# Performance work log

Measured on AMD Instinct MI355X. Metric: run time of the kernel, lower is better.

Reference implementation:

```python
import jax, jax.numpy as jnp
import numpy as np

B, S, D = 8, 4096, 192
MEM_READ, MEM_WRITE, MEM_READY = 156, 157, 158


def setup_inputs() -> dict:
    key = jax.random.key(0)
    ks = jax.random.split(key, 9)
    inp = {"x": jax.random.normal(ks[0], (B, S, D), dtype=jnp.float32)}
    names = ["Wq_r", "Wk_r", "Wv_r", "Wo_r", "Wq_w", "Wk_w", "Wv_w", "Wo_w"]
    for i, n in enumerate(names):
        inp[n] = jax.random.normal(ks[i + 1], (D, D), dtype=jnp.float32) * 0.02
    return inp


def _attention(x, Wq, Wk, Wv, Wo):
    # single-head, non-causal PureAttention: q/k/v = x @ W.T, softmax(qk^T/sqrt(D)) v, then W_o
    q = jnp.einsum('bsd,ed->bse', x, Wq)
    k = jnp.einsum('bsd,ed->bse', x, Wk)
    v = jnp.einsum('bsd,ed->bse', x, Wv)
    scale = jnp.asarray(1.0 / np.sqrt(D), x.dtype)
    scores = jnp.einsum('bqe,bke->bqk', q, k) * scale  # [B,S,S]
    attn = jax.nn.softmax(scores, axis=-1)
    o = jnp.einsum('bqk,bke->bqe', attn, v)
    return jnp.einsum('bse,oe->bso', o, Wo)


def reference(x, Wq_r, Wk_r, Wv_r, Wo_r, Wq_w, Wk_w, Wv_w, Wo_w):
    read_flag = x[:, 0, MEM_READ]    # [B]
    write_flag = x[:, 0, MEM_WRITE]  # [B]
    read_res = _attention(x, Wq_r, Wk_r, Wv_r, Wo_r)
    write_res = _attention(x, Wq_w, Wk_w, Wv_w, Wo_w)
    rg = read_flag[:, None, None]
    wg = write_flag[:, None, None]
    out = x + rg * (read_res - x) + wg * (write_res - x)
    out = out.at[:, :, MEM_READ].set(0.0)
    out = out.at[:, :, MEM_WRITE].set(0.0)
    ready = (read_flag + write_flag)[:, None]  # broadcast over seq
    out = out.at[:, :, MEM_READY].set(jnp.broadcast_to(ready, out.shape[:2]))
    return out
```

## Files before the change

kernel.cpp:

```cpp
#include <hip/hip_runtime.h>
#include <stdint.h>

#define B_ 8
#define S_ 4096
#define D_ 192
#define M_ (B_*S_)

typedef short v8s __attribute__((ext_vector_type(8)));
typedef float v4f __attribute__((ext_vector_type(4)));
typedef unsigned short v4us __attribute__((ext_vector_type(4)));

static __device__ __forceinline__ unsigned short f2bf(float f){
  union{float f; unsigned u;} v; v.f=f;
  unsigned u = v.u;
  unsigned r = (u + 0x7fffu + ((u>>16)&1u))>>16;
  return (unsigned short)r;
}
static __device__ __forceinline__ float fexp2(float x){
  return __builtin_amdgcn_exp2f(x);
}
static __device__ __forceinline__ unsigned cvtpk(float lo, float hi){
  unsigned r;
  asm("v_cvt_pk_bf16_f32 %0, %1, %2" : "=v"(r) : "v"(lo), "v"(hi));
  return r;
}

typedef const __attribute__((address_space(1))) unsigned int gu32;
typedef __attribute__((address_space(3))) unsigned int lu32;
#define GLL16(gp, lp) __builtin_amdgcn_global_load_lds((gu32*)(gp), (lu32*)(lp), 16, 0, 0)

__global__ void cvt_w_kernel(const float* w0,const float* w1,const float* w2,const float* w3,
                             const float* w4,const float* w5,const float* w6,const float* w7,
                             unsigned short* dst){
  int w = blockIdx.y;
  const float* src;
  switch(w){
    case 0: src=w0; break; case 1: src=w1; break; case 2: src=w2; break; case 3: src=w3; break;
    case 4: src=w4; break; case 5: src=w5; break; case 6: src=w6; break; default: src=w7; break;
  }
  int i = blockIdx.x*256 + threadIdx.x;
  float v = src[i];
  if(w==0 || w==4) v *= 0.10411754211316668f;
  dst[(size_t)w*36864 + i] = f2bf(v);
}

__global__ __launch_bounds__(256) void proj_kernel(
    const float* __restrict__ x, const unsigned short* __restrict__ Wb,
    unsigned short* __restrict__ QKV)
{
  __shared__ __align__(16) unsigned short Vstage[192*72];
  const size_t MD = (size_t)M_*D_;
  int tid = threadIdx.x;
  int wid = tid>>6, lane = tid&63;
  int lr = lane&15, lg = lane>>4, kb = lg*8;
  int m0 = blockIdx.x*64 + wid*16;
  int row = m0 + lr;

  v8s a[6];
  #pragma unroll
  for(int c=0;c<6;c++){
    const float* xp = &x[(size_t)row*D_ + c*32 + kb];
    float4 f0 = *(const float4*)xp;
    float4 f1 = *(const float4*)(xp+4);
    v8s t;
    t[0]=(short)f2bf(f0.x); t[1]=(short)f2bf(f0.y); t[2]=(short)f2bf(f0.z); t[3]=(short)f2bf(f0.w);
    t[4]=(short)f2bf(f1.x); t[5]=(short)f2bf(f1.y); t[6]=(short)f2bf(f1.z); t[7]=(short)f2bf(f1.w);
    a[c]=t;
  }
  int bidx = m0 / S_;
  int sb   = (blockIdx.x*64) % S_;
  int sloc = wid*16 + lg*4;

  for(int path=0; path<2; path++){
    unsigned short* dstQ = QKV + (size_t)path*3*MD;
    for(int which=0; which<2; which++){
      const unsigned short* W = Wb + (size_t)(path*4 + which)*36864;
      unsigned short* dst = which==0 ? dstQ : dstQ + MD;
      #pragma unroll
      for(int nt=0; nt<12; nt++){
        v4f acc = {0.f,0.f,0.f,0.f};
        int n = nt*16 + lr;
        #pragma unroll
        for(int c=0;c<6;c++){
          v8s bfr = *(const v8s*)&W[(size_t)n*D_ + c*32 + kb];
          acc = __builtin_amdgcn_mfma_f32_16x16x32_bf16(a[c], bfr, acc, 0,0,0);
        }
        int col = nt*16 + lr;
        int r0 = m0 + lg*4;
        #pragma unroll
        for(int r=0;r<4;r++) dst[(size_t)(r0+r)*D_ + col] = f2bf(acc[r]);
      }
    }
    {
      const unsigned short* W = Wb + (size_t)(path*4 + 2)*36864;
      #pragma unroll
      for(int nt=0; nt<12; nt++){
        v4f acc = {0.f,0.f,0.f,0.f};
        int n = nt*16 + lr;
        #pragma unroll
        for(int c=0;c<6;c++){
          v8s bfr = *(const v8s*)&W[(size_t)n*D_ + c*32 + kb];
          acc = __builtin_amdgcn_mfma_f32_16x16x32_bf16(a[c], bfr, acc, 0,0,0);
        }
        int col = nt*16 + lr;
        v4us pk;
        pk[0]=f2bf(acc[0]); pk[1]=f2bf(acc[1]); pk[2]=f2bf(acc[2]); pk[3]=f2bf(acc[3]);
        *(v4us*)&Vstage[col*72 + sloc] = pk;
      }
      __syncthreads();
      unsigned short* dstV = dstQ + 2*MD;
      size_t vg = (size_t)bidx*D_*S_ + sb;
      #pragma unroll
      for(int j=0;j<6;j++){
        int i = tid + j*256;
        int d = i>>3, s8 = (i&7)*8;
        *(v8s*)&dstV[vg + (size_t)d*S_ + s8] = *(const v8s*)&Vstage[d*72 + s8];
      }
      __syncthreads();
    }
  }
}

__global__ __launch_bounds__(512,3) void attn_kernel(unsigned short* __restrict__ QKV)
{
  __shared__ __align__(16) unsigned short Kb[2][32*192];
  __shared__ __align__(16) unsigned short Vb[3][192*32];

  int flat = blockIdx.x + 32*blockIdx.y + 256*blockIdx.z;
  int w = (flat&7)*64 + (flat>>3);
  int qi = w & 31;
  int b  = (w>>5) & 7;
  int z  = w>>8;

  const size_t MD = (size_t)M_*D_;
  size_t poff = (size_t)z*3*MD;
  const unsigned short* Q  = QKV + poff;
  const unsigned short* K  = QKV + poff + MD;
  const unsigned short* Vt = QKV + poff + 2*MD;
  unsigned short* O = QKV + poff;

  int q0 = qi*128;
  int tid = threadIdx.x, wid=tid>>6, lane=tid&63;
  int lr = lane&15, lg = lane>>4, kb = lg*8;
  size_t bbase = (size_t)b*S_*D_;
  const size_t vbase = (size_t)b*D_*S_;
  int qrow0 = q0 + wid*16;

  bool isK = wid < 4;
  int cb = (isK ? wid : wid-4)*3;
  int soff[3];
  #pragma unroll
  for(int j=0;j<3;j++){
    int pb = (cb+j)*1024 + lane*16;
    if(isK){
      int krow = pb/384, kin = pb%384;
      soff[j] = krow*192 + ((kin ^ ((krow&7)<<4))>>1);
    } else {
      int vrow = pb>>6,  vin = pb&63;
      soff[j] = vrow*4096 + ((vin ^ (((vrow>>1)&3)<<4))>>1);
    }
  }
  int xk = (lr&7)<<4;
  int kco[6];
  #pragma unroll
  for(int c=0;c<6;c++) kco[c] = ((c*64 + lg*16) ^ xk) >> 1;
  int vro = ((lg*16) ^ (((lr>>1)&3)<<4)) >> 1;

  v8s qf[6];
  {
    size_t qrow = bbase + (size_t)(qrow0 + lr)*D_;
    #pragma unroll
    for(int c=0;c<6;c++) qf[c] = *(const v8s*)&Q[qrow + c*32 + kb];
  }
  float lsum = 0.f;
  v4f oacc[12];
  #pragma unroll
  for(int e=0;e<12;e++) oacc[e] = (v4f){0.f,0.f,0.f,0.f};

  auto stage = [&](int t, int kbuf, int vbuf){
    if(isK){
      const unsigned short* kg = K + bbase + (size_t)t*6144;
      #pragma unroll
      for(int j=0;j<3;j++) GLL16(kg + soff[j], &Kb[kbuf][(cb+j)*512]);
    } else {
      const unsigned short* vg = Vt + vbase + (size_t)t*32;
      #pragma unroll
      for(int j=0;j<3;j++) GLL16(vg + soff[j], &Vb[vbuf][(cb+j)*512]);
    }
  };
  auto do_qk = [&](int kcur, v4f sacc[2]){
    __builtin_amdgcn_s_setprio(1);
    #pragma unroll
    for(int ct=0; ct<2; ct++){
      v4f s = {0.f,0.f,0.f,0.f};
      #pragma unroll
      for(int c=0;c<6;c++){
        v8s kf = *(const v8s*)&Kb[kcur][(ct*16+lr)*192 + kco[c]];
        s = __builtin_amdgcn_mfma_f32_16x16x32_bf16(kf, qf[c], s, 0,0,0);
      }
      sacc[ct]=s;
    }
    __builtin_amdgcn_s_setprio(0);
  };
  auto do_softmax = [&](v4f sacc[2], v8s& pa){
    float p00=fexp2(sacc[0][0]), p01=fexp2(sacc[0][1]);
    float p02=fexp2(sacc[0][2]), p03=fexp2(sacc[0][3]);
    float p10=fexp2(sacc[1][0]), p11=fexp2(sacc[1][1]);
    float p12=fexp2(sacc[1][2]), p13=fexp2(sacc[1][3]);
    lsum += ((p00+p01)+(p02+p03)) + ((p10+p11)+(p12+p13));
    unsigned X0=cvtpk(p00,p01), X1=cvtpk(p02,p03);
    unsigned Y0=cvtpk(p10,p11), Y1=cvtpk(p12,p13);
    asm("v_permlane32_swap_b32 %0, %1" : "+v"(Y0), "+v"(X0));
    asm("v_permlane32_swap_b32 %0, %1" : "+v"(Y1), "+v"(X1));
    asm("v_permlane16_swap_b32 %0, %1" : "+v"(Y0), "+v"(X0));
    asm("v_permlane16_swap_b32 %0, %1" : "+v"(Y1), "+v"(X1));
    union{ v8s s; unsigned w[4]; } u;
    u.w[0] = X0;  u.w[1] = X1;  u.w[2] = Y0;  u.w[3] = Y1;
    pa = u.s;
  };
  auto do_pv = [&](int vcur, v8s pa){
    __builtin_amdgcn_s_setprio(1);
    #pragma unroll
    for(int e=0;e<12;e++){
      v8s vbf = *(const v8s*)&Vb[vcur][(e*16+lr)*32 + vro];
      oacc[e] = __builtin_amdgcn_mfma_f32_16x16x32_bf16(pa, vbf, oacc[e], 0,0,0);
    }
    __builtin_amdgcn_s_setprio(0);
  };

  stage(0, 0, 0);
  asm volatile("s_waitcnt vmcnt(0)" ::: "memory");
  __syncthreads();

  v8s pa_prev;
  {
    v4f sacc[2];
    do_qk(0, sacc);
    stage(1, 1, 1);
    __builtin_amdgcn_sched_barrier(0);
    do_softmax(sacc, pa_prev);
  }

  for(int t=1; t<128; t++){
    asm volatile("s_waitcnt vmcnt(0)" ::: "memory");
    __syncthreads();
    v4f sacc[2];
    do_qk(t&1, sacc);
    if(t<127) stage(t+1, (t+1)&1, (t+1)%3);
    __builtin_amdgcn_sched_barrier(0);
    do_pv((t-1)%3, pa_prev);
    do_softmax(sacc, pa_prev);
  }
  do_pv(127%3, pa_prev);

  float ps = lsum;
  ps += __shfl_xor(ps, 16);
  ps += __shfl_xor(ps, 32);
  float iv = 1.0f/ps;
  float invr[4];
  #pragma unroll
  for(int r=0;r<4;r++) invr[r] = __shfl(iv, lg*4+r, 16);
  size_t orow0 = bbase + (size_t)(qrow0 + lg*4)*D_;
  #pragma unroll
  for(int e=0;e<12;e++){
    #pragma unroll
    for(int r=0;r<4;r++){
      O[orow0 + (size_t)r*D_ + e*16 + lr] = f2bf(oacc[e][r]*invr[r]);
    }
  }
}

__global__ __launch_bounds__(256) void final_kernel(
  const float* __restrict__ x,
  const unsigned short* __restrict__ Or,
  const unsigned short* __restrict__ Ow,
  const unsigned short* __restrict__ WoR,
  const unsigned short* __restrict__ WoW,
  float* __restrict__ out)
{
  int tid=threadIdx.x, wid=tid>>6, lane=tid&63;
  int lr=lane&15, lg=lane>>4, kb=lg*8;
  int m0 = blockIdx.x*64 + wid*16;
  int arow = m0 + lr;
  v8s ar[6], aw[6];
  #pragma unroll
  for(int c=0;c<6;c++){
    ar[c] = *(const v8s*)&Or[(size_t)arow*D_ + c*32 + kb];
    aw[c] = *(const v8s*)&Ow[(size_t)arow*D_ + c*32 + kb];
  }
  int bidx = m0 / S_;
  float rf = x[(size_t)bidx*S_*D_ + 156];
  float wf = x[(size_t)bidx*S_*D_ + 157];
  #pragma unroll
  for(int nt=0; nt<12; nt++){
    v4f accR={0.f,0.f,0.f,0.f}, accW={0.f,0.f,0.f,0.f};
    int n = nt*16 + lr;
    #pragma unroll
    for(int c=0;c<6;c++){
      v8s br = *(const v8s*)&WoR[(size_t)n*D_ + c*32 + kb];
      accR = __builtin_amdgcn_mfma_f32_16x16x32_bf16(ar[c], br, accR,0,0,0);
      v8s bw = *(const v8s*)&WoW[(size_t)n*D_ + c*32 + kb];
      accW = __builtin_amdgcn_mfma_f32_16x16x32_bf16(aw[c], bw, accW,0,0,0);
    }
    #pragma unroll
    for(int r=0;r<4;r++){
      int row = m0 + lg*4 + r;
      int col = nt*16 + lr;
      float xv = x[(size_t)row*D_ + col];
      float val = xv + rf*(accR[r]-xv) + wf*(accW[r]-xv);
      if(col==156||col==157) val = 0.f;
      else if(col==158) val = rf+wf;
      out[(size_t)row*D_ + col] = val;
    }
  }
}

extern "C" void kernel_launch(void* const* d_in, const int* in_sizes, int n_in,
                              void* d_out, int out_size, void* d_ws, size_t ws_size,
                              hipStream_t stream) {
  const float* x = (const float*)d_in[0];
  unsigned short* ws = (unsigned short*)d_ws;
  const size_t WSZ = 36864;
  const size_t MD  = (size_t)M_*D_;
  unsigned short* Wb  = ws;
  unsigned short* QKV = ws + 8*WSZ;

  cvt_w_kernel<<<dim3(144,8),256,0,stream>>>(
      (const float*)d_in[1],(const float*)d_in[2],(const float*)d_in[3],(const float*)d_in[4],
      (const float*)d_in[5],(const float*)d_in[6],(const float*)d_in[7],(const float*)d_in[8], Wb);

  proj_kernel<<<512,256,0,stream>>>(x, Wb, QKV);
  attn_kernel<<<dim3(32,8,2),512,0,stream>>>(QKV);
  final_kernel<<<512,256,0,stream>>>(x, QKV , QKV+3*MD ,
                                     Wb+3*WSZ, Wb+7*WSZ, (float*)d_out);
}
```

Baseline: 356.8 us.

## Switch attention Q/K/V and probabilities to FP8 MFMA

Projections now write Q, K and V as FP8 bytes, with the softmax scale split evenly across Wq and Wk. The attention kernel uses 16x16x32 FP8 MFMAs for both QK and PV, and repacks the softmax probabilities to FP8. This halves the Q/K/V memory traffic and LDS footprint and uses higher-throughput FP8 matrix instructions. The LDS staging is reorganised and outputs go to a separate bf16 buffer. The cost is a large loss of precision in the scores and probabilities, plus extra conversion work in softmax.

```diff
diff --git a/kernel.cpp b/kernel.cpp
--- a/kernel.cpp
+++ b/kernel.cpp
@@ -8,7 +8,6 @@
 
 typedef short v8s __attribute__((ext_vector_type(8)));
 typedef float v4f __attribute__((ext_vector_type(4)));
-typedef unsigned short v4us __attribute__((ext_vector_type(4)));
 
 static __device__ __forceinline__ unsigned short f2bf(float f){
   union{float f; unsigned u;} v; v.f=f;
@@ -23,6 +22,37 @@
   unsigned r;
   asm("v_cvt_pk_bf16_f32 %0, %1, %2" : "=v"(r) : "v"(lo), "v"(hi));
   return r;
+}
+static __device__ __forceinline__ float asf(unsigned u){
+  union{unsigned u; float f;} v; v.u=u; return v.f;
+}
+
+static __device__ __forceinline__ unsigned sw_fp8(float x){
+  union{float f; unsigned u;} v; v.f = x;
+  unsigned s = (v.u >> 24) & 0x80u;
+  float a = fabsf(x);
+  if (a < 0.001953125f) return s;
+  if (a >= 240.f) return s | 0x7Eu;
+  if (a < 0.015625f) {
+    int m = (int)(a*512.f + 0.5f); if(m>7) m=7;
+    return s | (unsigned)m;
+  }
+  int e = (int)((v.u >> 23) & 0xff) - 127;
+  unsigned mant = (v.u >> 20) & 0x7u;
+  unsigned rest = v.u & 0xFFFFFu;
+  if (rest > 0x80000u || (rest == 0x80000u && (mant&1u))) mant++;
+  unsigned ee = (unsigned)(e + 7);
+  if (mant == 8u){ mant = 0u; ee++; }
+  return s | (ee<<3) | mant;
+}
+template<bool HI>
+static __device__ __forceinline__ unsigned pk8(float a, float b, unsigned old){
+#if __has_builtin(__builtin_amdgcn_cvt_pk_fp8_f32)
+  return __builtin_amdgcn_cvt_pk_fp8_f32(a, b, old, HI);
+#else
+  unsigned p = sw_fp8(a) | (sw_fp8(b)<<8);
+  return HI ? ((old & 0x0000FFFFu) | (p<<16)) : ((old & 0xFFFF0000u) | p);
+#endif
 }
 
 typedef const __attribute__((address_space(1))) unsigned int gu32;
@@ -40,16 +70,16 @@
   }
   int i = blockIdx.x*256 + threadIdx.x;
   float v = src[i];
-  if(w==0 || w==4) v *= 0.10411754211316668f;
+  if(w==0 || w==4 || w==1 || w==5) v *= 0.32267249f;
   dst[(size_t)w*36864 + i] = f2bf(v);
 }
 
 __global__ __launch_bounds__(256) void proj_kernel(
     const float* __restrict__ x, const unsigned short* __restrict__ Wb,
-    unsigned short* __restrict__ QKV)
+    unsigned char* __restrict__ QKV8)
 {
-  __shared__ __align__(16) unsigned short Vstage[192*72];
-  const size_t MD = (size_t)M_*D_;
+  __shared__ __align__(16) unsigned char Vstage[192*80];
+  const size_t MDB = (size_t)M_*D_;
   int tid = threadIdx.x;
   int wid = tid>>6, lane = tid&63;
   int lr = lane&15, lg = lane>>4, kb = lg*8;
@@ -72,10 +102,10 @@
   int sloc = wid*16 + lg*4;
 
   for(int path=0; path<2; path++){
-    unsigned short* dstQ = QKV + (size_t)path*3*MD;
+    unsigned char* dstQ = QKV8 + (size_t)path*3*MDB;
     for(int which=0; which<2; which++){
       const unsigned short* W = Wb + (size_t)(path*4 + which)*36864;
-      unsigned short* dst = which==0 ? dstQ : dstQ + MD;
+      unsigned char* dst = which==0 ? dstQ : dstQ + MDB;
       #pragma unroll
       for(int nt=0; nt<12; nt++){
         v4f acc = {0.f,0.f,0.f,0.f};
@@ -88,7 +118,10 @@
         int col = nt*16 + lr;
         int r0 = m0 + lg*4;
         #pragma unroll
-        for(int r=0;r<4;r++) dst[(size_t)(r0+r)*D_ + col] = f2bf(acc[r]);
+        for(int r=0;r<4;r++){
+          unsigned p = pk8<false>(acc[r], 0.f, 0u);
+          dst[(size_t)(r0+r)*D_ + col] = (unsigned char)(p & 0xFF);
+        }
       }
     }
     {
@@ -103,28 +136,29 @@
           acc = __builtin_amdgcn_mfma_f32_16x16x32_bf16(a[c], bfr, acc, 0,0,0);
         }
         int col = nt*16 + lr;
-        v4us pk;
-        pk[0]=f2bf(acc[0]); pk[1]=f2bf(acc[1]); pk[2]=f2bf(acc[2]); pk[3]=f2bf(acc[3]);
-        *(v4us*)&Vstage[col*72 + sloc] = pk;
+        unsigned pk4 = pk8<false>(acc[0], acc[1], 0u);
+        pk4 = pk8<true>(acc[2], acc[3], pk4);
+        *(unsigned*)&Vstage[col*80 + sloc] = pk4;
       }
       __syncthreads();
-      unsigned short* dstV = dstQ + 2*MD;
+      unsigned char* dstV = dstQ + 2*MDB;
       size_t vg = (size_t)bidx*D_*S_ + sb;
       #pragma unroll
-      for(int j=0;j<6;j++){
+      for(int j=0;j<3;j++){
         int i = tid + j*256;
-        int d = i>>3, s8 = (i&7)*8;
-        *(v8s*)&dstV[vg + (size_t)d*S_ + s8] = *(const v8s*)&Vstage[d*72 + s8];
+        int d = i>>2, ci = (i&3)*16;
+        *(v8s*)&dstV[vg + (size_t)d*S_ + ci] = *(const v8s*)&Vstage[d*80 + ci];
       }
       __syncthreads();
     }
   }
 }
 
-__global__ __launch_bounds__(512,3) void attn_kernel(unsigned short* __restrict__ QKV)
+__global__ __launch_bounds__(512,3) void attn_kernel(const unsigned char* __restrict__ QKV8,
+                                                     unsigned short* __restrict__ Ob)
 {
-  __shared__ __align__(16) unsigned short Kb[2][32*192];
-  __shared__ __align__(16) unsigned short Vb[3][192*32];
+  __shared__ __align__(16) unsigned char KL[2*8192];
+  __shared__ __align__(16) unsigned char VL[3*9216];
 
   int flat = blockIdx.x + 32*blockIdx.y + 256*blockIdx.z;
   int w = (flat&7)*64 + (flat>>3);
@@ -132,45 +166,41 @@
   int b  = (w>>5) & 7;
   int z  = w>>8;
 
-  const size_t MD = (size_t)M_*D_;
-  size_t poff = (size_t)z*3*MD;
-  const unsigned short* Q  = QKV + poff;
-  const unsigned short* K  = QKV + poff + MD;
-  const unsigned short* Vt = QKV + poff + 2*MD;
-  unsigned short* O = QKV + poff;
+  const size_t MDB = (size_t)M_*D_;
+  const unsigned char* Q8 = QKV8 + (size_t)z*3*MDB;
+  const unsigned char* K8 = Q8 + MDB;
+  const unsigned char* V8 = Q8 + 2*MDB;
+  unsigned short* O = Ob + (size_t)z*M_*D_;
 
   int q0 = qi*128;
   int tid = threadIdx.x, wid=tid>>6, lane=tid&63;
-  int lr = lane&15, lg = lane>>4, kb = lg*8;
-  size_t bbase = (size_t)b*S_*D_;
-  const size_t vbase = (size_t)b*D_*S_;
+  int lr = lane&15, lg = lane>>4;
+  size_t bK = (size_t)b*S_*D_;
+  size_t bV = (size_t)b*D_*S_;
   int qrow0 = q0 + wid*16;
 
-  bool isK = wid < 4;
-  int cb = (isK ? wid : wid-4)*3;
-  int soff[3];
-  #pragma unroll
-  for(int j=0;j<3;j++){
-    int pb = (cb+j)*1024 + lane*16;
-    if(isK){
-      int krow = pb/384, kin = pb%384;
-      soff[j] = krow*192 + ((kin ^ ((krow&7)<<4))>>1);
-    } else {
-      int vrow = pb>>6,  vin = pb&63;
-      soff[j] = vrow*4096 + ((vin ^ (((vrow>>1)&3)<<4))>>1);
-    }
-  }
-  int xk = (lr&7)<<4;
-  int kco[6];
-  #pragma unroll
-  for(int c=0;c<6;c++) kco[c] = ((c*64 + lg*16) ^ xk) >> 1;
-  int vro = ((lg*16) ^ (((lr>>1)&3)<<4)) >> 1;
-
-  v8s qf[6];
+  int krow = tid>>4, kpc = (tid&15)<<4;
+  int kg = kpc ^ ((krow&7)<<4);
+  int kSrc = krow*192 + (kg<192 ? kg : 176);
+  int kLds = tid*16;
+  int vd0 = tid/3,        vq0 = (tid%3)<<4;
+  int vSrc0 = vd0*S_ + (vq0<32 ? vq0 : 16);
+  int vLds0 = tid*16;
+  int vc1 = tid+512;
+  int vd1 = vc1/3,        vq1 = (vc1%3)<<4;
+  int vSrc1 = vd1*S_ + (vq1<32 ? vq1 : 16);
+  int vLds1 = vc1*16;
+  bool v2 = tid < 64;
+
+  int kro[6];
+  #pragma unroll
+  for(int c=0;c<6;c++) kro[c] = (c*32 + lg*8) ^ ((lr&7)<<4);
+
+  long qf8[6];
   {
-    size_t qrow = bbase + (size_t)(qrow0 + lr)*D_;
-    #pragma unroll
-    for(int c=0;c<6;c++) qf[c] = *(const v8s*)&Q[qrow + c*32 + kb];
+    const unsigned char* qp = Q8 + bK + (size_t)(qrow0 + lr)*D_;
+    #pragma unroll
+    for(int c=0;c<6;c++) qf8[c] = *(const long*)(qp + c*32 + lg*8);
   }
   float lsum = 0.f;
   v4f oacc[12];
@@ -178,31 +208,29 @@
   for(int e=0;e<12;e++) oacc[e] = (v4f){0.f,0.f,0.f,0.f};
 
   auto stage = [&](int t, int kbuf, int vbuf){
-    if(isK){
-      const unsigned short* kg = K + bbase + (size_t)t*6144;
-      #pragma unroll
-      for(int j=0;j<3;j++) GLL16(kg + soff[j], &Kb[kbuf][(cb+j)*512]);
-    } else {
-      const unsigned short* vg = Vt + vbase + (size_t)t*32;
-      #pragma unroll
-      for(int j=0;j<3;j++) GLL16(vg + soff[j], &Vb[vbuf][(cb+j)*512]);
-    }
+    const unsigned char* Kg = K8 + bK + (size_t)t*6144;
+    const unsigned char* Vg = V8 + bV + (size_t)t*32;
+    GLL16(Kg + kSrc, KL + kbuf*8192 + kLds);
+    GLL16(Vg + vSrc0, VL + vbuf*9216 + vLds0);
+    if(v2) GLL16(Vg + vSrc1, VL + vbuf*9216 + vLds1);
   };
   auto do_qk = [&](int kcur, v4f sacc[2]){
+    const unsigned char* KB = KL + kcur*8192;
     __builtin_amdgcn_s_setprio(1);
     #pragma unroll
     for(int ct=0; ct<2; ct++){
       v4f s = {0.f,0.f,0.f,0.f};
+      const unsigned char* rb = KB + (ct*16+lr)*256;
       #pragma unroll
       for(int c=0;c<6;c++){
-        v8s kf = *(const v8s*)&Kb[kcur][(ct*16+lr)*192 + kco[c]];
-        s = __builtin_amdgcn_mfma_f32_16x16x32_bf16(kf, qf[c], s, 0,0,0);
+        long kf8 = *(const long*)(rb + kro[c]);
+        s = __builtin_amdgcn_mfma_f32_16x16x32_fp8_fp8(kf8, qf8[c], s, 0,0,0);
       }
       sacc[ct]=s;
     }
     __builtin_amdgcn_s_setprio(0);
   };
-  auto do_softmax = [&](v4f sacc[2], v8s& pa){
+  auto do_softmax = [&](v4f sacc[2], long& pa8){
     float p00=fexp2(sacc[0][0]), p01=fexp2(sacc[0][1]);
     float p02=fexp2(sacc[0][2]), p03=fexp2(sacc[0][3]);
     float p10=fexp2(sacc[1][0]), p11=fexp2(sacc[1][1]);
@@ -214,16 +242,21 @@
     asm("v_permlane32_swap_b32 %0, %1" : "+v"(Y1), "+v"(X1));
     asm("v_permlane16_swap_b32 %0, %1" : "+v"(Y0), "+v"(X0));
     asm("v_permlane16_swap_b32 %0, %1" : "+v"(Y1), "+v"(X1));
-    union{ v8s s; unsigned w[4]; } u;
-    u.w[0] = X0;  u.w[1] = X1;  u.w[2] = Y0;  u.w[3] = Y1;
-    pa = u.s;
+    float e0 = asf(X0<<16), e1 = asf(X0 & 0xffff0000u);
+    float e2 = asf(X1<<16), e3 = asf(X1 & 0xffff0000u);
+    float e4 = asf(Y0<<16), e5 = asf(Y0 & 0xffff0000u);
+    float e6 = asf(Y1<<16), e7 = asf(Y1 & 0xffff0000u);
+    unsigned lo = pk8<false>(e0,e1,0u); lo = pk8<true>(e2,e3,lo);
+    unsigned hi = pk8<false>(e4,e5,0u); hi = pk8<true>(e6,e7,hi);
+    pa8 = (long)(((unsigned long long)hi<<32) | (unsigned long long)lo);
   };
-  auto do_pv = [&](int vcur, v8s pa){
+  auto do_pv = [&](int vcur, long pa8){
+    const unsigned char* VB = VL + vcur*9216;
     __builtin_amdgcn_s_setprio(1);
     #pragma unroll
     for(int e=0;e<12;e++){
-      v8s vbf = *(const v8s*)&Vb[vcur][(e*16+lr)*32 + vro];
-      oacc[e] = __builtin_amdgcn_mfma_f32_16x16x32_bf16(pa, vbf, oacc[e], 0,0,0);
+      long vb8 = *(const long*)(VB + (e*16+lr)*48 + lg*8);
+      oacc[e] = __builtin_amdgcn_mfma_f32_16x16x32_fp8_fp8(pa8, vb8, oacc[e], 0,0,0);
     }
     __builtin_amdgcn_s_setprio(0);
   };
@@ -232,7 +265,7 @@
   asm volatile("s_waitcnt vmcnt(0)" ::: "memory");
   __syncthreads();
 
-  v8s pa_prev;
+  long pa_prev;
   {
     v4f sacc[2];
     do_qk(0, sacc);
@@ -260,7 +293,7 @@
   float invr[4];
   #pragma unroll
   for(int r=0;r<4;r++) invr[r] = __shfl(iv, lg*4+r, 16);
-  size_t orow0 = bbase + (size_t)(qrow0 + lg*4)*D_;
+  size_t orow0 = ((size_t)b*S_ + qrow0 + lg*4)*D_;
   #pragma unroll
   for(int e=0;e<12;e++){
     #pragma unroll
@@ -319,18 +352,19 @@
                               void* d_out, int out_size, void* d_ws, size_t ws_size,
                               hipStream_t stream) {
   const float* x = (const float*)d_in[0];
-  unsigned short* ws = (unsigned short*)d_ws;
+  char* wsb = (char*)d_ws;
   const size_t WSZ = 36864;
-  const size_t MD  = (size_t)M_*D_;
-  unsigned short* Wb  = ws;
-  unsigned short* QKV = ws + 8*WSZ;
+  const size_t MDB = (size_t)M_*D_;
+  unsigned short* Wb = (unsigned short*)wsb;
+  unsigned char*  Q8 = (unsigned char*)(wsb + 8*WSZ*2);
+  unsigned short* Ob = (unsigned short*)(wsb + 8*WSZ*2 + 2*3*MDB);
 
   cvt_w_kernel<<<dim3(144,8),256,0,stream>>>(
       (const float*)d_in[1],(const float*)d_in[2],(const float*)d_in[3],(const float*)d_in[4],
       (const float*)d_in[5],(const float*)d_in[6],(const float*)d_in[7],(const float*)d_in[8], Wb);
 
-  proj_kernel<<<512,256,0,stream>>>(x, Wb, QKV);
-  attn_kernel<<<dim3(32,8,2),512,0,stream>>>(QKV);
-  final_kernel<<<512,256,0,stream>>>(x, QKV , QKV+3*MD ,
+  proj_kernel<<<512,256,0,stream>>>(x, Wb, Q8);
+  attn_kernel<<<dim3(32,8,2),512,0,stream>>>(Q8, Ob);
+  final_kernel<<<512,256,0,stream>>>(x, Ob, Ob + (size_t)M_*D_,
                                      Wb+3*WSZ, Wb+7*WSZ, (float*)d_out);
 }
```

Measured after the change: 367.9 us. 3.1% more time.
